# Optimization experiments

Measured on AMD Instinct MI355X. Metric: run time of the kernel, lower is better.

Reference implementation:

```python
import jax, jax.numpy as jnp
import numpy as np

C = 256   # hidden_size (in_channels)
V = 97    # VOC_SIZE + 1
T = 32    # encoder time steps
N = 4096  # batch of text instances


def setup_inputs() -> dict:
    key = jax.random.key(0)
    ks = jax.random.split(key, 10)
    s = lambda k, shape: jax.random.normal(k, shape, dtype=jnp.float32) * 0.05
    return {
        "input": jax.random.randint(ks[0], (N,), 0, V),
        "hidden": s(ks[1], (1, N, C)),
        "encoder_outputs": s(ks[2], (T, N, C)),
        "emb": s(ks[3], (V, C)),
        "combine_w": s(ks[4], (C, 2 * C)), "combine_b": jnp.zeros((C,), jnp.float32),
        "vat_w": s(ks[5], (1, C)), "vat_b": jnp.zeros((1,), jnp.float32),
        "gru_w_ih": s(ks[6], (3 * C, C)), "gru_w_hh": s(ks[7], (3 * C, C)),
        "gru_b_ih": jnp.zeros((3 * C,), jnp.float32), "gru_b_hh": jnp.zeros((3 * C,), jnp.float32),
        "out_w": s(ks[8], (V, C)), "out_b": jnp.zeros((V,), jnp.float32),
    }


def reference(input, hidden, encoder_outputs, emb, combine_w, combine_b,
              vat_w, vat_b, gru_w_ih, gru_w_hh, gru_b_ih, gru_b_hh,
              out_w, out_b):
    # Embedding lookup (dropout = identity in eval mode)
    embedded = emb[input]                                   # [N, C]

    # Bahdanau additive attention: vat(tanh(hidden + enc))
    alpha = jnp.tanh(hidden + encoder_outputs)              # [T, N, C]
    scores = jnp.einsum('tnc,c->nt', alpha, vat_w[0]) + vat_b[0]  # [N, T]
    attn = jax.nn.softmax(scores, axis=1)                   # [N, T]
    applied = jnp.einsum('nt,tnc->nc', attn, encoder_outputs)     # [N, C]

    # Combine + relu
    x = jnp.concatenate([embedded, applied], axis=1) @ combine_w.T + combine_b  # [N, C]
    x = jax.nn.relu(x)

    # Single-step GRU cell (PyTorch gate ordering: r, z, n)
    h = hidden[0]                                           # [N, C]
    gi = x @ gru_w_ih.T + gru_b_ih                          # [N, 3C]
    gh = h @ gru_w_hh.T + gru_b_hh                          # [N, 3C]
    ir, iz, i_n = jnp.split(gi, 3, axis=1)
    hr, hz, h_n = jnp.split(gh, 3, axis=1)
    r = jax.nn.sigmoid(ir + hr)
    z = jax.nn.sigmoid(iz + hz)
    n = jnp.tanh(i_n + r * h_n)
    h_new = (1.0 - z) * n + z * h                           # [N, C]

    out = jax.nn.log_softmax(h_new @ out_w.T + out_b, axis=1)  # [N, V]
    return out, h_new[None, :, :], attn[:, None, :]
```

## Files before the change

### kernel.cpp

```cpp
#include <hip/hip_runtime.h>

typedef unsigned short u16;
typedef unsigned int u32;
using bf16x8 = __attribute__((ext_vector_type(8))) __bf16;
using f32x4  = __attribute__((ext_vector_type(4))) float;

__device__ __forceinline__ u16 f2bf(float f) {
  union { float f; unsigned int i; } v; v.f = f;
  unsigned int r = v.i + 0x7fffu + ((v.i >> 16) & 1u);
  return (u16)(r >> 16);
}
__device__ __forceinline__ void cvt8(u16* dst, const float* src) {
  float4 a0 = *reinterpret_cast<const float4*>(src);
  float4 a1 = *reinterpret_cast<const float4*>(src + 4);
  dst[0] = f2bf(a0.x); dst[1] = f2bf(a0.y); dst[2] = f2bf(a0.z); dst[3] = f2bf(a0.w);
  dst[4] = f2bf(a1.x); dst[5] = f2bf(a1.y); dst[6] = f2bf(a1.z); dst[7] = f2bf(a1.w);
}
__device__ __forceinline__ float ftanh(float x) {
  float e = __expf(2.f * x);
  return 1.f - 2.f / (e + 1.f);
}
__device__ __forceinline__ float fsigm(float x) {
  return 1.f / (1.f + __expf(-x));
}
__device__ __forceinline__ float ptanh(float x) {
  const float c1 = -0.3333333333f, c2 = 0.1333333333f, c3 = -0.0539682540f;
  float t = x * x;
  float r = __builtin_fmaf(__builtin_fmaf(c3, t, c2), t, c1);
  return __builtin_fmaf(x * t, r, x);
}

__global__ __launch_bounds__(256) void k_prep(
    const float* __restrict__ cw, const float* __restrict__ wih,
    const float* __restrict__ whh, const float* __restrict__ ow,
    u16* __restrict__ Wc, u16* __restrict__ Wi,
    u16* __restrict__ Wh, u16* __restrict__ Wo)
{
  int id = blockIdx.x * 256 + threadIdx.x;
  u16 tmp[8];
  if (id < 16384) {
    cvt8(tmp, &cw[id * 8]);
    *reinterpret_cast<uint4*>(&Wc[id * 8]) = *reinterpret_cast<const uint4*>(tmp);
  } else if (id < 40960) {
    int c = id - 16384;
    cvt8(tmp, &wih[c * 8]);
    *reinterpret_cast<uint4*>(&Wi[c * 8]) = *reinterpret_cast<const uint4*>(tmp);
  } else if (id < 65536) {
    int c = id - 40960;
    cvt8(tmp, &whh[c * 8]);
    *reinterpret_cast<uint4*>(&Wh[c * 8]) = *reinterpret_cast<const uint4*>(tmp);
  } else {
    int c = id - 65536;
    int row = c >> 5, col = (c & 31) * 8;
    if (row < 97) {
      cvt8(tmp, &ow[row * 256 + col]);
    } else {
      #pragma unroll
      for (int i = 0; i < 8; ++i) tmp[i] = 0;
    }
    *reinterpret_cast<uint4*>(&Wo[c * 8]) = *reinterpret_cast<const uint4*>(tmp);
  }
}

__global__ __launch_bounds__(512) void k_fused(
    const float* __restrict__ enc, const float* __restrict__ hid,
    const float* __restrict__ vw,  const float* __restrict__ emb,
    const int* __restrict__ inp,
    const u16* __restrict__ Wc, const u16* __restrict__ Wi,
    const u16* __restrict__ Wh, const u16* __restrict__ Wo,
    const float* __restrict__ cb, const float* __restrict__ bih,
    const float* __restrict__ bhh, const float* __restrict__ bo,
    float* __restrict__ out_logits, float* __restrict__ out_h,
    float* __restrict__ out_attn)
{
  __shared__ __attribute__((aligned(16))) u16 Ac_s[16 * 16 * 40];
  __shared__ __attribute__((aligned(16))) u16 Hb_s[8 * 16 * 40];
  __shared__ __attribute__((aligned(16))) u16 X_s [8 * 16 * 40];
  __shared__ __attribute__((aligned(16))) u16 Hn_s[8 * 16 * 40];
  __shared__ float es_s[16 * 33];
  __shared__ float l_s[16];
  __shared__ float L_s[16 * 113];

  const int tid = threadIdx.x;
  const int n0  = blockIdx.x * 16;

  {
    const int nl = tid >> 5;
    const int cg = tid & 31;
    const int c0 = cg * 8;
    const int n  = n0 + nl;

    const float4 h0 = *reinterpret_cast<const float4*>(&hid[n * 256 + c0]);
    const float4 h1 = *reinterpret_cast<const float4*>(&hid[n * 256 + c0 + 4]);
    const float4 w0 = *reinterpret_cast<const float4*>(&vw[c0]);
    const float4 w1 = *reinterpret_cast<const float4*>(&vw[c0 + 4]);

    {
      u16 t8[8];
      t8[0]=f2bf(h0.x); t8[1]=f2bf(h0.y); t8[2]=f2bf(h0.z); t8[3]=f2bf(h0.w);
      t8[4]=f2bf(h1.x); t8[5]=f2bf(h1.y); t8[6]=f2bf(h1.z); t8[7]=f2bf(h1.w);
      *reinterpret_cast<uint4*>(&Hb_s[((cg >> 2) * 16 + nl) * 40 + (cg & 3) * 8]) =
        *reinterpret_cast<const uint4*>(t8);
    }
    {
      u16 t8[8];
      cvt8(t8, &emb[(size_t)inp[n] * 256 + c0]);
      *reinterpret_cast<uint4*>(&Ac_s[((cg >> 2) * 16 + nl) * 40 + (cg & 3) * 8]) =
        *reinterpret_cast<const uint4*>(t8);
    }

    float a0=0.f,a1=0.f,a2=0.f,a3=0.f,a4=0.f,a5=0.f,a6=0.f,a7=0.f;
    float l = 0.f;

    const float* ep = &enc[(size_t)n * 256 + c0];
    #pragma unroll 4
    for (int t = 0; t < 32; ++t) {
      const float* p = ep + (size_t)t * 1048576;
      float4 e0 = *reinterpret_cast<const float4*>(p);
      float4 e1 = *reinterpret_cast<const float4*>(p + 4);

      float s;
      s  = ptanh(h0.x + e0.x) * w0.x;
      s  = __builtin_fmaf(ptanh(h0.y + e0.y), w0.y, s);
      s  = __builtin_fmaf(ptanh(h0.z + e0.z), w0.z, s);
      s  = __builtin_fmaf(ptanh(h0.w + e0.w), w0.w, s);
      s  = __builtin_fmaf(ptanh(h1.x + e1.x), w1.x, s);
      s  = __builtin_fmaf(ptanh(h1.y + e1.y), w1.y, s);
      s  = __builtin_fmaf(ptanh(h1.z + e1.z), w1.z, s);
      s  = __builtin_fmaf(ptanh(h1.w + e1.w), w1.w, s);
      #pragma unroll
      for (int k = 16; k >= 1; k >>= 1) s += __shfl_xor(s, k, 64);

      float e = __expf(s);
      l += e;
      a0 = __builtin_fmaf(e, e0.x, a0); a1 = __builtin_fmaf(e, e0.y, a1);
      a2 = __builtin_fmaf(e, e0.z, a2); a3 = __builtin_fmaf(e, e0.w, a3);
      a4 = __builtin_fmaf(e, e1.x, a4); a5 = __builtin_fmaf(e, e1.y, a5);
      a6 = __builtin_fmaf(e, e1.z, a6); a7 = __builtin_fmaf(e, e1.w, a7);
      if (cg == 0) es_s[nl * 33 + t] = e;
    }

    {
      float rl = 1.f / l;
      u16 t8[8];
      t8[0]=f2bf(a0*rl); t8[1]=f2bf(a1*rl); t8[2]=f2bf(a2*rl); t8[3]=f2bf(a3*rl);
      t8[4]=f2bf(a4*rl); t8[5]=f2bf(a5*rl); t8[6]=f2bf(a6*rl); t8[7]=f2bf(a7*rl);
      *reinterpret_cast<uint4*>(&Ac_s[((8 + (cg >> 2)) * 16 + nl) * 40 + (cg & 3) * 8]) =
        *reinterpret_cast<const uint4*>(t8);
    }
    if (cg == 0) l_s[nl] = l;
  }
  __syncthreads();

  {
    int n2 = tid >> 5, t2 = tid & 31;
    out_attn[(size_t)(n0 + n2) * 32 + t2] = es_s[n2 * 33 + t2] / l_s[n2];
  }

  const int wave = tid >> 6, lane = tid & 63;
  const int lr = lane & 15, quad = lane >> 4;

  {
    f32x4 accB[2] = {};
    const u16* wp = &Wc[(size_t)(wave * 32 + lr) * 512 + quad * 8];
    #pragma unroll
    for (int kt = 0; kt < 16; ++kt) {
      bf16x8 aF = *reinterpret_cast<const bf16x8*>(&Ac_s[(kt * 16 + lr) * 40 + quad * 8]);
      bf16x8 b0 = *reinterpret_cast<const bf16x8*>(&wp[kt * 32]);
      bf16x8 b1 = *reinterpret_cast<const bf16x8*>(&wp[16 * 512 + kt * 32]);
      accB[0] = __builtin_amdgcn_mfma_f32_16x16x32_bf16(aF, b0, accB[0], 0, 0, 0);
      accB[1] = __builtin_amdgcn_mfma_f32_16x16x32_bf16(aF, b1, accB[1], 0, 0, 0);
    }
    #pragma unroll
    for (int sn = 0; sn < 2; ++sn) {
      int col = wave * 32 + sn * 16 + lr;
      float bv = cb[col];
      #pragma unroll
      for (int r = 0; r < 4; ++r) {
        float v = fmaxf(accB[sn][r] + bv, 0.f);
        X_s[((col >> 5) * 16 + quad * 4 + r) * 40 + (col & 31)] = f2bf(v);
      }
    }
  }
  __syncthreads();

  {
    f32x4 aI[3][2] = {};
    f32x4 aH[3][2] = {};
    const int c0w = wave * 32;
    const u16* baseI = &Wi[(size_t)(c0w + lr) * 256 + quad * 8];
    const u16* baseH = &Wh[(size_t)(c0w + lr) * 256 + quad * 8];
    #pragma unroll
    for (int kt = 0; kt < 8; ++kt) {
      bf16x8 xF = *reinterpret_cast<const bf16x8*>(&X_s [(kt * 16 + lr) * 40 + quad * 8]);
      bf16x8 hF = *reinterpret_cast<const bf16x8*>(&Hb_s[(kt * 16 + lr) * 40 + quad * 8]);
      #pragma unroll
      for (int g = 0; g < 3; ++g) {
        #pragma unroll
        for (int sn = 0; sn < 2; ++sn) {
          const size_t off = (size_t)(g * 256 + sn * 16) * 256 + kt * 32;
          bf16x8 bI = *reinterpret_cast<const bf16x8*>(&baseI[off]);
          bf16x8 bH = *reinterpret_cast<const bf16x8*>(&baseH[off]);
          aI[g][sn] = __builtin_amdgcn_mfma_f32_16x16x32_bf16(xF, bI, aI[g][sn], 0, 0, 0);
          aH[g][sn] = __builtin_amdgcn_mfma_f32_16x16x32_bf16(hF, bH, aH[g][sn], 0, 0, 0);
        }
      }
    }
    #pragma unroll
    for (int sn = 0; sn < 2; ++sn) {
      int gc = c0w + sn * 16 + lr;
      float b_ir = bih[gc],       b_hr = bhh[gc];
      float b_iz = bih[256 + gc], b_hz = bhh[256 + gc];
      float b_in = bih[512 + gc], b_hn = bhh[512 + gc];
      #pragma unroll
      for (int r = 0; r < 4; ++r) {
        int row = quad * 4 + r;
        float rg = fsigm(aI[0][sn][r] + b_ir + aH[0][sn][r] + b_hr);
        float zg = fsigm(aI[1][sn][r] + b_iz + aH[1][sn][r] + b_hz);
        float ng = ftanh(aI[2][sn][r] + b_in + rg * (aH[2][sn][r] + b_hn));
        float hv = hid[(size_t)(n0 + row) * 256 + gc];
        float hn = (1.f - zg) * ng + zg * hv;
        out_h[(size_t)(n0 + row) * 256 + gc] = hn;
        Hn_s[((gc >> 5) * 16 + row) * 40 + (gc & 31)] = f2bf(hn);
      }
    }
  }
  __syncthreads();

  if (wave < 7) {
    f32x4 accO = {};
    const u16* wp = &Wo[(size_t)(wave * 16 + lr) * 256 + quad * 8];
    #pragma unroll
    for (int kt = 0; kt < 8; ++kt) {
      bf16x8 aF = *reinterpret_cast<const bf16x8*>(&Hn_s[(kt * 16 + lr) * 40 + quad * 8]);
      bf16x8 bF = *reinterpret_cast<const bf16x8*>(&wp[kt * 32]);
      accO = __builtin_amdgcn_mfma_f32_16x16x32_bf16(aF, bF, accO, 0, 0, 0);
    }
    int col = wave * 16 + lr;
    if (col < 97) {
      float bv = bo[col];
      #pragma unroll
      for (int r = 0; r < 4; ++r)
        L_s[(quad * 4 + r) * 113 + col] = accO[r] + bv;
    }
  }
  __syncthreads();

  {
    int row = tid >> 5, p = tid & 31;
    float m = -1e30f, l = 0.f;
    for (int c = p; c < 97; c += 32) {
      float v = L_s[row * 113 + c];
      if (v > m) { l = l * __expf(m - v) + 1.f; m = v; }
      else l += __expf(v - m);
    }
    #pragma unroll
    for (int k = 16; k >= 1; k >>= 1) {
      float m2 = __shfl_xor(m, k, 64);
      float l2 = __shfl_xor(l, k, 64);
      if (m2 > m) { l = l * __expf(m - m2) + l2; m = m2; }
      else l += l2 * __expf(m2 - m);
    }
    float lz = m + __logf(l);
    for (int c = p; c < 97; c += 32)
      out_logits[(size_t)(n0 + row) * 97 + c] = L_s[row * 113 + c] - lz;
  }
}

extern "C" void kernel_launch(void* const* d_in, const int* in_sizes, int n_in,
                              void* d_out, int out_size, void* d_ws, size_t ws_size,
                              hipStream_t stream) {
  const int*   inp = (const int*)d_in[0];
  const float* hid = (const float*)d_in[1];
  const float* enc = (const float*)d_in[2];
  const float* emb = (const float*)d_in[3];
  const float* cw  = (const float*)d_in[4];
  const float* cb  = (const float*)d_in[5];
  const float* vw  = (const float*)d_in[6];
  const float* wih = (const float*)d_in[8];
  const float* whh = (const float*)d_in[9];
  const float* bih = (const float*)d_in[10];
  const float* bhh = (const float*)d_in[11];
  const float* ow  = (const float*)d_in[12];
  const float* ob  = (const float*)d_in[13];

  float* out        = (float*)d_out;
  float* out_logits = out;
  float* out_h      = out + 4096 * 97;
  float* out_attn   = out_h + 4096 * 256;

  u16* Wc = (u16*)d_ws;
  u16* Wi = Wc + 131072;
  u16* Wh = Wi + 196608;
  u16* Wo = Wh + 196608;

  k_prep<<<270, 256, 0, stream>>>(cw, wih, whh, ow, Wc, Wi, Wh, Wo);
  k_fused<<<256, 512, 0, stream>>>(enc, hid, vw, emb, inp,
                                   Wc, Wi, Wh, Wo, cb, bih, bhh, ob,
                                   out_logits, out_h, out_attn);
}
```

Before: 253.5 us.

## Halve rows per block to eight and double grid, aliasing shared memory

Each block now handles 8 batch rows instead of 16, with one wave per row in the attention stage, and the grid doubles to 512 blocks. The point is more blocks across CUs and better latency hiding in the memory-bound encoder scan. Shared buffers are aliased into one region to cut LDS use, which needs an extra barrier before X_s is written. In exchange, the 16-row MFMA tiles are half padding, so matrix work is wasted, and each weight matrix is read from L2 twice as many times overall.

```diff
diff --git a/kernel.cpp b/kernel.cpp
--- a/kernel.cpp
+++ b/kernel.cpp
@@ -73,92 +73,83 @@
     float* __restrict__ out_logits, float* __restrict__ out_h,
     float* __restrict__ out_attn)
 {
-  __shared__ __attribute__((aligned(16))) u16 Ac_s[16 * 16 * 40];
-  __shared__ __attribute__((aligned(16))) u16 Hb_s[8 * 16 * 40];
-  __shared__ __attribute__((aligned(16))) u16 X_s [8 * 16 * 40];
-  __shared__ __attribute__((aligned(16))) u16 Hn_s[8 * 16 * 40];
-  __shared__ float es_s[16 * 33];
-  __shared__ float l_s[16];
-  __shared__ float L_s[16 * 113];
+  __shared__ __attribute__((aligned(16))) u16 smem[15360];
+  u16* Ac_s = smem;
+  u16* X_s  = smem;
+  u16* Hn_s = smem + 5120;
+  u16* Hb_s = smem + 10240;
+  float* L_s = reinterpret_cast<float*>(smem + 10240);
+  __shared__ float es_s[8 * 33];
+  __shared__ float l_s[8];
 
   const int tid = threadIdx.x;
-  const int n0  = blockIdx.x * 16;
-
-  {
-    const int nl = tid >> 5;
-    const int cg = tid & 31;
-    const int c0 = cg * 8;
-    const int n  = n0 + nl;
-
-    const float4 h0 = *reinterpret_cast<const float4*>(&hid[n * 256 + c0]);
-    const float4 h1 = *reinterpret_cast<const float4*>(&hid[n * 256 + c0 + 4]);
-    const float4 w0 = *reinterpret_cast<const float4*>(&vw[c0]);
-    const float4 w1 = *reinterpret_cast<const float4*>(&vw[c0 + 4]);
+  const int n0  = blockIdx.x * 8;
+  const int wv  = tid >> 6;
+  const int ln  = tid & 63;
+
+  {
+    const int c0 = ln * 4;
+    const int n  = n0 + wv;
+    const int kt = ln >> 3;
+    const int cc = (ln & 7) * 4;
+
+    const float4 h = *reinterpret_cast<const float4*>(&hid[(size_t)n * 256 + c0]);
+    const float4 w = *reinterpret_cast<const float4*>(&vw[c0]);
 
     {
-      u16 t8[8];
-      t8[0]=f2bf(h0.x); t8[1]=f2bf(h0.y); t8[2]=f2bf(h0.z); t8[3]=f2bf(h0.w);
-      t8[4]=f2bf(h1.x); t8[5]=f2bf(h1.y); t8[6]=f2bf(h1.z); t8[7]=f2bf(h1.w);
-      *reinterpret_cast<uint4*>(&Hb_s[((cg >> 2) * 16 + nl) * 40 + (cg & 3) * 8]) =
-        *reinterpret_cast<const uint4*>(t8);
+      u16 t4[4];
+      t4[0]=f2bf(h.x); t4[1]=f2bf(h.y); t4[2]=f2bf(h.z); t4[3]=f2bf(h.w);
+      *reinterpret_cast<uint2*>(&Hb_s[(kt * 16 + wv) * 40 + cc]) =
+        *reinterpret_cast<const uint2*>(t4);
     }
     {
-      u16 t8[8];
-      cvt8(t8, &emb[(size_t)inp[n] * 256 + c0]);
-      *reinterpret_cast<uint4*>(&Ac_s[((cg >> 2) * 16 + nl) * 40 + (cg & 3) * 8]) =
-        *reinterpret_cast<const uint4*>(t8);
-    }
-
-    float a0=0.f,a1=0.f,a2=0.f,a3=0.f,a4=0.f,a5=0.f,a6=0.f,a7=0.f;
+      const float4 em = *reinterpret_cast<const float4*>(&emb[(size_t)inp[n] * 256 + c0]);
+      u16 t4[4];
+      t4[0]=f2bf(em.x); t4[1]=f2bf(em.y); t4[2]=f2bf(em.z); t4[3]=f2bf(em.w);
+      *reinterpret_cast<uint2*>(&Ac_s[(kt * 16 + wv) * 40 + cc]) =
+        *reinterpret_cast<const uint2*>(t4);
+    }
+
+    float a0=0.f, a1=0.f, a2=0.f, a3=0.f;
     float l = 0.f;
 
     const float* ep = &enc[(size_t)n * 256 + c0];
     #pragma unroll 4
     for (int t = 0; t < 32; ++t) {
-      const float* p = ep + (size_t)t * 1048576;
-      float4 e0 = *reinterpret_cast<const float4*>(p);
-      float4 e1 = *reinterpret_cast<const float4*>(p + 4);
+      const float4 e = *reinterpret_cast<const float4*>(ep + (size_t)t * 1048576);
 
       float s;
-      s  = ptanh(h0.x + e0.x) * w0.x;
-      s  = __builtin_fmaf(ptanh(h0.y + e0.y), w0.y, s);
-      s  = __builtin_fmaf(ptanh(h0.z + e0.z), w0.z, s);
-      s  = __builtin_fmaf(ptanh(h0.w + e0.w), w0.w, s);
-      s  = __builtin_fmaf(ptanh(h1.x + e1.x), w1.x, s);
-      s  = __builtin_fmaf(ptanh(h1.y + e1.y), w1.y, s);
-      s  = __builtin_fmaf(ptanh(h1.z + e1.z), w1.z, s);
-      s  = __builtin_fmaf(ptanh(h1.w + e1.w), w1.w, s);
-      #pragma unroll
-      for (int k = 16; k >= 1; k >>= 1) s += __shfl_xor(s, k, 64);
-
-      float e = __expf(s);
-      l += e;
-      a0 = __builtin_fmaf(e, e0.x, a0); a1 = __builtin_fmaf(e, e0.y, a1);
-      a2 = __builtin_fmaf(e, e0.z, a2); a3 = __builtin_fmaf(e, e0.w, a3);
-      a4 = __builtin_fmaf(e, e1.x, a4); a5 = __builtin_fmaf(e, e1.y, a5);
-      a6 = __builtin_fmaf(e, e1.z, a6); a7 = __builtin_fmaf(e, e1.w, a7);
-      if (cg == 0) es_s[nl * 33 + t] = e;
+      s  = ptanh(h.x + e.x) * w.x;
+      s  = __builtin_fmaf(ptanh(h.y + e.y), w.y, s);
+      s  = __builtin_fmaf(ptanh(h.z + e.z), w.z, s);
+      s  = __builtin_fmaf(ptanh(h.w + e.w), w.w, s);
+      #pragma unroll
+      for (int k = 32; k >= 1; k >>= 1) s += __shfl_xor(s, k, 64);
+
+      float ex = __expf(s);
+      l += ex;
+      a0 = __builtin_fmaf(ex, e.x, a0); a1 = __builtin_fmaf(ex, e.y, a1);
+      a2 = __builtin_fmaf(ex, e.z, a2); a3 = __builtin_fmaf(ex, e.w, a3);
+      if (ln == 0) es_s[wv * 33 + t] = ex;
     }
 
     {
       float rl = 1.f / l;
-      u16 t8[8];
-      t8[0]=f2bf(a0*rl); t8[1]=f2bf(a1*rl); t8[2]=f2bf(a2*rl); t8[3]=f2bf(a3*rl);
-      t8[4]=f2bf(a4*rl); t8[5]=f2bf(a5*rl); t8[6]=f2bf(a6*rl); t8[7]=f2bf(a7*rl);
-      *reinterpret_cast<uint4*>(&Ac_s[((8 + (cg >> 2)) * 16 + nl) * 40 + (cg & 3) * 8]) =
-        *reinterpret_cast<const uint4*>(t8);
-    }
-    if (cg == 0) l_s[nl] = l;
-  }
-  __syncthreads();
-
-  {
+      u16 t4[4];
+      t4[0]=f2bf(a0*rl); t4[1]=f2bf(a1*rl); t4[2]=f2bf(a2*rl); t4[3]=f2bf(a3*rl);
+      *reinterpret_cast<uint2*>(&Ac_s[((8 + kt) * 16 + wv) * 40 + cc]) =
+        *reinterpret_cast<const uint2*>(t4);
+    }
+    if (ln == 0) l_s[wv] = l;
+  }
+  __syncthreads();
+
+  if (tid < 256) {
     int n2 = tid >> 5, t2 = tid & 31;
     out_attn[(size_t)(n0 + n2) * 32 + t2] = es_s[n2 * 33 + t2] / l_s[n2];
   }
 
-  const int wave = tid >> 6, lane = tid & 63;
-  const int lr = lane & 15, quad = lane >> 4;
+  const int wave = wv, lr = ln & 15, quad = ln >> 4;
 
   {
     f32x4 accB[2] = {};
@@ -171,14 +162,17 @@
       accB[0] = __builtin_amdgcn_mfma_f32_16x16x32_bf16(aF, b0, accB[0], 0, 0, 0);
       accB[1] = __builtin_amdgcn_mfma_f32_16x16x32_bf16(aF, b1, accB[1], 0, 0, 0);
     }
-    #pragma unroll
-    for (int sn = 0; sn < 2; ++sn) {
-      int col = wave * 32 + sn * 16 + lr;
-      float bv = cb[col];
-      #pragma unroll
-      for (int r = 0; r < 4; ++r) {
-        float v = fmaxf(accB[sn][r] + bv, 0.f);
-        X_s[((col >> 5) * 16 + quad * 4 + r) * 40 + (col & 31)] = f2bf(v);
+    __syncthreads();
+    if (quad < 2) {
+      #pragma unroll
+      for (int sn = 0; sn < 2; ++sn) {
+        int col = wave * 32 + sn * 16 + lr;
+        float bv = cb[col];
+        #pragma unroll
+        for (int r = 0; r < 4; ++r) {
+          float v = fmaxf(accB[sn][r] + bv, 0.f);
+          X_s[((col >> 5) * 16 + quad * 4 + r) * 40 + (col & 31)] = f2bf(v);
+        }
       }
     }
   }
@@ -206,22 +200,24 @@
         }
       }
     }
-    #pragma unroll
-    for (int sn = 0; sn < 2; ++sn) {
-      int gc = c0w + sn * 16 + lr;
-      float b_ir = bih[gc],       b_hr = bhh[gc];
-      float b_iz = bih[256 + gc], b_hz = bhh[256 + gc];
-      float b_in = bih[512 + gc], b_hn = bhh[512 + gc];
-      #pragma unroll
-      for (int r = 0; r < 4; ++r) {
-        int row = quad * 4 + r;
-        float rg = fsigm(aI[0][sn][r] + b_ir + aH[0][sn][r] + b_hr);
-        float zg = fsigm(aI[1][sn][r] + b_iz + aH[1][sn][r] + b_hz);
-        float ng = ftanh(aI[2][sn][r] + b_in + rg * (aH[2][sn][r] + b_hn));
-        float hv = hid[(size_t)(n0 + row) * 256 + gc];
-        float hn = (1.f - zg) * ng + zg * hv;
-        out_h[(size_t)(n0 + row) * 256 + gc] = hn;
-        Hn_s[((gc >> 5) * 16 + row) * 40 + (gc & 31)] = f2bf(hn);
+    if (quad < 2) {
+      #pragma unroll
+      for (int sn = 0; sn < 2; ++sn) {
+        int gc = c0w + sn * 16 + lr;
+        float b_ir = bih[gc],       b_hr = bhh[gc];
+        float b_iz = bih[256 + gc], b_hz = bhh[256 + gc];
+        float b_in = bih[512 + gc], b_hn = bhh[512 + gc];
+        #pragma unroll
+        for (int r = 0; r < 4; ++r) {
+          int row = quad * 4 + r;
+          float rg = fsigm(aI[0][sn][r] + b_ir + aH[0][sn][r] + b_hr);
+          float zg = fsigm(aI[1][sn][r] + b_iz + aH[1][sn][r] + b_hz);
+          float ng = ftanh(aI[2][sn][r] + b_in + rg * (aH[2][sn][r] + b_hn));
+          float hv = hid[(size_t)(n0 + row) * 256 + gc];
+          float hn = (1.f - zg) * ng + zg * hv;
+          out_h[(size_t)(n0 + row) * 256 + gc] = hn;
+          Hn_s[((gc >> 5) * 16 + row) * 40 + (gc & 31)] = f2bf(hn);
+        }
       }
     }
   }
@@ -237,7 +233,7 @@
       accO = __builtin_amdgcn_mfma_f32_16x16x32_bf16(aF, bF, accO, 0, 0, 0);
     }
     int col = wave * 16 + lr;
-    if (col < 97) {
+    if (col < 97 && quad < 2) {
       float bv = bo[col];
       #pragma unroll
       for (int r = 0; r < 4; ++r)
@@ -247,22 +243,22 @@
   __syncthreads();
 
   {
-    int row = tid >> 5, p = tid & 31;
+    int row = wv;
     float m = -1e30f, l = 0.f;
-    for (int c = p; c < 97; c += 32) {
+    for (int c = ln; c < 97; c += 64) {
       float v = L_s[row * 113 + c];
       if (v > m) { l = l * __expf(m - v) + 1.f; m = v; }
       else l += __expf(v - m);
     }
     #pragma unroll
-    for (int k = 16; k >= 1; k >>= 1) {
+    for (int k = 32; k >= 1; k >>= 1) {
       float m2 = __shfl_xor(m, k, 64);
       float l2 = __shfl_xor(l, k, 64);
       if (m2 > m) { l = l * __expf(m - m2) + l2; m = m2; }
       else l += l2 * __expf(m2 - m);
     }
     float lz = m + __logf(l);
-    for (int c = p; c < 97; c += 32)
+    for (int c = ln; c < 97; c += 64)
       out_logits[(size_t)(n0 + row) * 97 + c] = L_s[row * 113 + c] - lz;
   }
 }
@@ -295,7 +291,7 @@
   u16* Wo = Wh + 196608;
 
   k_prep<<<270, 256, 0, stream>>>(cw, wih, whh, ow, Wc, Wi, Wh, Wo);
-  k_fused<<<256, 512, 0, stream>>>(enc, hid, vw, emb, inp,
+  k_fused<<<512, 512, 0, stream>>>(enc, hid, vw, emb, inp,
                                    Wc, Wi, Wh, Wo, cb, bih, bhh, ob,
                                    out_logits, out_h, out_attn);
 }
```

Measured after the change: 280.9 us. 10.8% more time.

## Software-pipeline global loads with register ring buffers and request two blocks per CU

Applied to the files above, without the earlier changes.

Adds explicit register prefetching throughout the fused kernel. The encoder loop loads four time steps ahead, and each MFMA GEMM stage (combine, GRU input/hidden, output projection) streams its weight fragments through a 4-deep register ring. The GRU accumulators are flattened into a 12-entry array, and hidden-state values and biases are loaded before the MMA loop. Launch bounds now ask for 2 blocks per CU, which caps registers per thread and may cause spills.

```diff
diff --git a/kernel.cpp b/kernel.cpp
--- a/kernel.cpp
+++ b/kernel.cpp
@@ -62,7 +62,7 @@
   }
 }
 
-__global__ __launch_bounds__(512) void k_fused(
+__global__ __launch_bounds__(512, 2) void k_fused(
     const float* __restrict__ enc, const float* __restrict__ hid,
     const float* __restrict__ vw,  const float* __restrict__ emb,
     const int* __restrict__ inp,
@@ -90,8 +90,8 @@
     const int c0 = cg * 8;
     const int n  = n0 + nl;
 
-    const float4 h0 = *reinterpret_cast<const float4*>(&hid[n * 256 + c0]);
-    const float4 h1 = *reinterpret_cast<const float4*>(&hid[n * 256 + c0 + 4]);
+    const float4 h0 = *reinterpret_cast<const float4*>(&hid[(size_t)n * 256 + c0]);
+    const float4 h1 = *reinterpret_cast<const float4*>(&hid[(size_t)n * 256 + c0 + 4]);
     const float4 w0 = *reinterpret_cast<const float4*>(&vw[c0]);
     const float4 w1 = *reinterpret_cast<const float4*>(&vw[c0 + 4]);
 
@@ -113,31 +113,44 @@
     float l = 0.f;
 
     const float* ep = &enc[(size_t)n * 256 + c0];
-    #pragma unroll 4
-    for (int t = 0; t < 32; ++t) {
-      const float* p = ep + (size_t)t * 1048576;
-      float4 e0 = *reinterpret_cast<const float4*>(p);
-      float4 e1 = *reinterpret_cast<const float4*>(p + 4);
-
-      float s;
-      s  = ptanh(h0.x + e0.x) * w0.x;
-      s  = __builtin_fmaf(ptanh(h0.y + e0.y), w0.y, s);
-      s  = __builtin_fmaf(ptanh(h0.z + e0.z), w0.z, s);
-      s  = __builtin_fmaf(ptanh(h0.w + e0.w), w0.w, s);
-      s  = __builtin_fmaf(ptanh(h1.x + e1.x), w1.x, s);
-      s  = __builtin_fmaf(ptanh(h1.y + e1.y), w1.y, s);
-      s  = __builtin_fmaf(ptanh(h1.z + e1.z), w1.z, s);
-      s  = __builtin_fmaf(ptanh(h1.w + e1.w), w1.w, s);
-      #pragma unroll
-      for (int k = 16; k >= 1; k >>= 1) s += __shfl_xor(s, k, 64);
-
-      float e = __expf(s);
-      l += e;
-      a0 = __builtin_fmaf(e, e0.x, a0); a1 = __builtin_fmaf(e, e0.y, a1);
-      a2 = __builtin_fmaf(e, e0.z, a2); a3 = __builtin_fmaf(e, e0.w, a3);
-      a4 = __builtin_fmaf(e, e1.x, a4); a5 = __builtin_fmaf(e, e1.y, a5);
-      a6 = __builtin_fmaf(e, e1.z, a6); a7 = __builtin_fmaf(e, e1.w, a7);
-      if (cg == 0) es_s[nl * 33 + t] = e;
+    float4 E0[4], E1[4];
+    #pragma unroll
+    for (int i = 0; i < 4; ++i) {
+      const float* p = ep + (size_t)i * 1048576;
+      E0[i] = *reinterpret_cast<const float4*>(p);
+      E1[i] = *reinterpret_cast<const float4*>(p + 4);
+    }
+    #pragma unroll
+    for (int tb = 0; tb < 32; tb += 4) {
+      #pragma unroll
+      for (int i = 0; i < 4; ++i) {
+        const int t = tb + i;
+        float4 e0 = E0[i], e1 = E1[i];
+        if (tb < 28) {
+          const float* p = ep + (size_t)(t + 4) * 1048576;
+          E0[i] = *reinterpret_cast<const float4*>(p);
+          E1[i] = *reinterpret_cast<const float4*>(p + 4);
+        }
+        float s;
+        s  = ptanh(h0.x + e0.x) * w0.x;
+        s  = __builtin_fmaf(ptanh(h0.y + e0.y), w0.y, s);
+        s  = __builtin_fmaf(ptanh(h0.z + e0.z), w0.z, s);
+        s  = __builtin_fmaf(ptanh(h0.w + e0.w), w0.w, s);
+        s  = __builtin_fmaf(ptanh(h1.x + e1.x), w1.x, s);
+        s  = __builtin_fmaf(ptanh(h1.y + e1.y), w1.y, s);
+        s  = __builtin_fmaf(ptanh(h1.z + e1.z), w1.z, s);
+        s  = __builtin_fmaf(ptanh(h1.w + e1.w), w1.w, s);
+        #pragma unroll
+        for (int k = 16; k >= 1; k >>= 1) s += __shfl_xor(s, k, 64);
+
+        float e = __expf(s);
+        l += e;
+        a0 = __builtin_fmaf(e, e0.x, a0); a1 = __builtin_fmaf(e, e0.y, a1);
+        a2 = __builtin_fmaf(e, e0.z, a2); a3 = __builtin_fmaf(e, e0.w, a3);
+        a4 = __builtin_fmaf(e, e1.x, a4); a5 = __builtin_fmaf(e, e1.y, a5);
+        a6 = __builtin_fmaf(e, e1.z, a6); a7 = __builtin_fmaf(e, e1.w, a7);
+        if (cg == 0) es_s[nl * 33 + t] = e;
+      }
     }
 
     {
@@ -163,18 +176,32 @@
   {
     f32x4 accB[2] = {};
     const u16* wp = &Wc[(size_t)(wave * 32 + lr) * 512 + quad * 8];
-    #pragma unroll
-    for (int kt = 0; kt < 16; ++kt) {
-      bf16x8 aF = *reinterpret_cast<const bf16x8*>(&Ac_s[(kt * 16 + lr) * 40 + quad * 8]);
-      bf16x8 b0 = *reinterpret_cast<const bf16x8*>(&wp[kt * 32]);
-      bf16x8 b1 = *reinterpret_cast<const bf16x8*>(&wp[16 * 512 + kt * 32]);
-      accB[0] = __builtin_amdgcn_mfma_f32_16x16x32_bf16(aF, b0, accB[0], 0, 0, 0);
-      accB[1] = __builtin_amdgcn_mfma_f32_16x16x32_bf16(aF, b1, accB[1], 0, 0, 0);
+    float bv0 = cb[wave * 32 + lr];
+    float bv1 = cb[wave * 32 + 16 + lr];
+
+    bf16x8 ring[4];
+    #pragma unroll
+    for (int i = 0; i < 4; ++i) {
+      int kt = i >> 1, half = i & 1;
+      ring[i] = *reinterpret_cast<const bf16x8*>(&wp[half * 16 * 512 + kt * 32]);
+    }
+    bf16x8 aF = {};
+    #pragma unroll
+    for (int s = 0; s < 32; ++s) {
+      const int kt = s >> 1, half = s & 1;
+      bf16x8 bF = ring[s & 3];
+      if (s + 4 < 32) {
+        int kt2 = (s + 4) >> 1, h2 = (s + 4) & 1;
+        ring[s & 3] = *reinterpret_cast<const bf16x8*>(&wp[h2 * 16 * 512 + kt2 * 32]);
+      }
+      if (half == 0)
+        aF = *reinterpret_cast<const bf16x8*>(&Ac_s[(kt * 16 + lr) * 40 + quad * 8]);
+      accB[half] = __builtin_amdgcn_mfma_f32_16x16x32_bf16(aF, bF, accB[half], 0, 0, 0);
     }
     #pragma unroll
     for (int sn = 0; sn < 2; ++sn) {
       int col = wave * 32 + sn * 16 + lr;
-      float bv = cb[col];
+      float bv = sn ? bv1 : bv0;
       #pragma unroll
       for (int r = 0; r < 4; ++r) {
         float v = fmaxf(accB[sn][r] + bv, 0.f);
@@ -185,41 +212,69 @@
   __syncthreads();
 
   {
-    f32x4 aI[3][2] = {};
-    f32x4 aH[3][2] = {};
     const int c0w = wave * 32;
     const u16* baseI = &Wi[(size_t)(c0w + lr) * 256 + quad * 8];
     const u16* baseH = &Wh[(size_t)(c0w + lr) * 256 + quad * 8];
-    #pragma unroll
-    for (int kt = 0; kt < 8; ++kt) {
-      bf16x8 xF = *reinterpret_cast<const bf16x8*>(&X_s [(kt * 16 + lr) * 40 + quad * 8]);
-      bf16x8 hF = *reinterpret_cast<const bf16x8*>(&Hb_s[(kt * 16 + lr) * 40 + quad * 8]);
-      #pragma unroll
-      for (int g = 0; g < 3; ++g) {
-        #pragma unroll
-        for (int sn = 0; sn < 2; ++sn) {
-          const size_t off = (size_t)(g * 256 + sn * 16) * 256 + kt * 32;
-          bf16x8 bI = *reinterpret_cast<const bf16x8*>(&baseI[off]);
-          bf16x8 bH = *reinterpret_cast<const bf16x8*>(&baseH[off]);
-          aI[g][sn] = __builtin_amdgcn_mfma_f32_16x16x32_bf16(xF, bI, aI[g][sn], 0, 0, 0);
-          aH[g][sn] = __builtin_amdgcn_mfma_f32_16x16x32_bf16(hF, bH, aH[g][sn], 0, 0, 0);
-        }
-      }
-    }
+
+    float b_ir[2], b_hr[2], b_iz[2], b_hz[2], b_in[2], b_hn[2], hv[2][4];
     #pragma unroll
     for (int sn = 0; sn < 2; ++sn) {
       int gc = c0w + sn * 16 + lr;
-      float b_ir = bih[gc],       b_hr = bhh[gc];
-      float b_iz = bih[256 + gc], b_hz = bhh[256 + gc];
-      float b_in = bih[512 + gc], b_hn = bhh[512 + gc];
+      b_ir[sn] = bih[gc];       b_hr[sn] = bhh[gc];
+      b_iz[sn] = bih[256 + gc]; b_hz[sn] = bhh[256 + gc];
+      b_in[sn] = bih[512 + gc]; b_hn[sn] = bhh[512 + gc];
+      #pragma unroll
+      for (int r = 0; r < 4; ++r) {
+        int row = (quad & 1) * 4 + r + (quad >> 1) * 8;
+        hv[sn][r] = hid[(size_t)(n0 + ((quad * 4 + r) & 15)) * 256 + gc];
+      }
+    }
+
+    f32x4 accC[12] = {};
+    bf16x8 ring[4];
+    #pragma unroll
+    for (int i = 0; i < 4; ++i) {
+      const int g = i >> 2, sn = (i >> 1) & 1, mat = i & 1;
+      const u16* base = mat ? baseH : baseI;
+      ring[i] = *reinterpret_cast<const bf16x8*>(&base[(size_t)(g * 256 + sn * 16) * 256]);
+    }
+    bf16x8 xF = {}, hF = {};
+    #pragma unroll
+    for (int s = 0; s < 96; ++s) {
+      const int kt = s / 12, j = s % 12;
+      const int mat = j & 1;
+      bf16x8 bF = ring[s & 3];
+      if (s + 4 < 96) {
+        const int s2 = s + 4, kt2 = s2 / 12, j2 = s2 % 12;
+        const int g2 = j2 >> 2, sn2 = (j2 >> 1) & 1, m2 = j2 & 1;
+        const u16* base = m2 ? baseH : baseI;
+        ring[s & 3] = *reinterpret_cast<const bf16x8*>(
+            &base[(size_t)(g2 * 256 + sn2 * 16) * 256 + kt2 * 32]);
+      }
+      if (j == 0) {
+        xF = *reinterpret_cast<const bf16x8*>(&X_s [(kt * 16 + lr) * 40 + quad * 8]);
+        hF = *reinterpret_cast<const bf16x8*>(&Hb_s[(kt * 16 + lr) * 40 + quad * 8]);
+      }
+      accC[j] = __builtin_amdgcn_mfma_f32_16x16x32_bf16(mat ? hF : xF, bF, accC[j], 0, 0, 0);
+    }
+
+    #pragma unroll
+    for (int sn = 0; sn < 2; ++sn) {
+      int gc = c0w + sn * 16 + lr;
       #pragma unroll
       for (int r = 0; r < 4; ++r) {
         int row = quad * 4 + r;
-        float rg = fsigm(aI[0][sn][r] + b_ir + aH[0][sn][r] + b_hr);
-        float zg = fsigm(aI[1][sn][r] + b_iz + aH[1][sn][r] + b_hz);
-        float ng = ftanh(aI[2][sn][r] + b_in + rg * (aH[2][sn][r] + b_hn));
-        float hv = hid[(size_t)(n0 + row) * 256 + gc];
-        float hn = (1.f - zg) * ng + zg * hv;
+        float aIr = accC[(0 << 2) | (sn << 1) | 0][r];
+        float aHr = accC[(0 << 2) | (sn << 1) | 1][r];
+        float aIz = accC[(1 << 2) | (sn << 1) | 0][r];
+        float aHz = accC[(1 << 2) | (sn << 1) | 1][r];
+        float aIn = accC[(2 << 2) | (sn << 1) | 0][r];
+        float aHn = accC[(2 << 2) | (sn << 1) | 1][r];
+        float rg = fsigm(aIr + b_ir[sn] + aHr + b_hr[sn]);
+        float zg = fsigm(aIz + b_iz[sn] + aHz + b_hz[sn]);
+        float ng = ftanh(aIn + b_in[sn] + rg * (aHn + b_hn[sn]));
+        float hvv = hv[sn][r];
+        float hn = (1.f - zg) * ng + zg * hvv;
         out_h[(size_t)(n0 + row) * 256 + gc] = hn;
         Hn_s[((gc >> 5) * 16 + row) * 40 + (gc & 31)] = f2bf(hn);
       }
@@ -230,10 +285,16 @@
   if (wave < 7) {
     f32x4 accO = {};
     const u16* wp = &Wo[(size_t)(wave * 16 + lr) * 256 + quad * 8];
+    bf16x8 ring[4];
+    #pragma unroll
+    for (int i = 0; i < 4; ++i)
+      ring[i] = *reinterpret_cast<const bf16x8*>(&wp[i * 32]);
     #pragma unroll
     for (int kt = 0; kt < 8; ++kt) {
+      bf16x8 bF = ring[kt & 3];
+      if (kt + 4 < 8)
+        ring[kt & 3] = *reinterpret_cast<const bf16x8*>(&wp[(kt + 4) * 32]);
       bf16x8 aF = *reinterpret_cast<const bf16x8*>(&Hn_s[(kt * 16 + lr) * 40 + quad * 8]);
-      bf16x8 bF = *reinterpret_cast<const bf16x8*>(&wp[kt * 32]);
       accO = __builtin_amdgcn_mfma_f32_16x16x32_bf16(aF, bF, accO, 0, 0, 0);
     }
     int col = wave * 16 + lr;
```

New measurement: 273.4 us. +7.9%, slower.

## Split attention into a separate per-row kernel with many more blocks

Applied to the files above, without the earlier changes.

Moves the attention stage out of the fused kernel into its own kernel that launches one 256-thread block per batch row, with each of four waves handling eight time steps. The previous version ran only 256 blocks. The new kernel writes the combined embedding and attention-applied vector in bf16 to a workspace buffer. A second kernel loads that buffer and runs the GEMM/GRU/output stages. This gives the memory-bound attention read far more parallelism for latency hiding, at the cost of an extra kernel launch and a global round-trip for the combined activations.

```diff
diff --git a/kernel.cpp b/kernel.cpp
--- a/kernel.cpp
+++ b/kernel.cpp
@@ -62,100 +62,91 @@
   }
 }
 
-__global__ __launch_bounds__(512) void k_fused(
+__global__ __launch_bounds__(256) void k_attn(
     const float* __restrict__ enc, const float* __restrict__ hid,
     const float* __restrict__ vw,  const float* __restrict__ emb,
     const int* __restrict__ inp,
+    float* __restrict__ out_attn, u16* __restrict__ Acomb)
+{
+  __shared__ float a_s[4][256];
+  __shared__ float es_s[32];
+  __shared__ float l_s[4];
+
+  const int n   = blockIdx.x;
+  const int tid = threadIdx.x;
+  const int w   = tid >> 6;
+  const int ln  = tid & 63;
+  const int c0  = ln * 4;
+
+  const float4 h  = *reinterpret_cast<const float4*>(&hid[(size_t)n * 256 + c0]);
+  const float4 wv = *reinterpret_cast<const float4*>(&vw[c0]);
+
+  float a0 = 0.f, a1 = 0.f, a2 = 0.f, a3 = 0.f, l = 0.f;
+  const float* ep = &enc[(size_t)n * 256 + c0];
+
+  #pragma unroll
+  for (int j = 0; j < 8; ++j) {
+    const int t = w * 8 + j;
+    const float4 e = *reinterpret_cast<const float4*>(ep + (size_t)t * 1048576);
+    float s;
+    s = ptanh(h.x + e.x) * wv.x;
+    s = __builtin_fmaf(ptanh(h.y + e.y), wv.y, s);
+    s = __builtin_fmaf(ptanh(h.z + e.z), wv.z, s);
+    s = __builtin_fmaf(ptanh(h.w + e.w), wv.w, s);
+    #pragma unroll
+    for (int k = 32; k >= 1; k >>= 1) s += __shfl_xor(s, k, 64);
+    float ex = __expf(s);
+    l += ex;
+    a0 = __builtin_fmaf(ex, e.x, a0); a1 = __builtin_fmaf(ex, e.y, a1);
+    a2 = __builtin_fmaf(ex, e.z, a2); a3 = __builtin_fmaf(ex, e.w, a3);
+    if (ln == 0) es_s[t] = ex;
+  }
+
+  *reinterpret_cast<float4*>(&a_s[w][c0]) = make_float4(a0, a1, a2, a3);
+  if (ln == 0) l_s[w] = l;
+  __syncthreads();
+
+  {
+    const int c = tid;
+    float lt = (l_s[0] + l_s[1]) + (l_s[2] + l_s[3]);
+    float at = (a_s[0][c] + a_s[1][c]) + (a_s[2][c] + a_s[3][c]);
+    Acomb[(size_t)n * 512 + 256 + c] = f2bf(at / lt);
+    float em = emb[(size_t)inp[n] * 256 + c];
+    Acomb[(size_t)n * 512 + c] = f2bf(em);
+    if (c < 32) out_attn[(size_t)n * 32 + c] = es_s[c] / lt;
+  }
+}
+
+__global__ __launch_bounds__(512) void k_rest(
+    const float* __restrict__ hid, const u16* __restrict__ Acomb,
     const u16* __restrict__ Wc, const u16* __restrict__ Wi,
     const u16* __restrict__ Wh, const u16* __restrict__ Wo,
     const float* __restrict__ cb, const float* __restrict__ bih,
     const float* __restrict__ bhh, const float* __restrict__ bo,
-    float* __restrict__ out_logits, float* __restrict__ out_h,
-    float* __restrict__ out_attn)
+    float* __restrict__ out_logits, float* __restrict__ out_h)
 {
   __shared__ __attribute__((aligned(16))) u16 Ac_s[16 * 16 * 40];
   __shared__ __attribute__((aligned(16))) u16 Hb_s[8 * 16 * 40];
   __shared__ __attribute__((aligned(16))) u16 X_s [8 * 16 * 40];
   __shared__ __attribute__((aligned(16))) u16 Hn_s[8 * 16 * 40];
-  __shared__ float es_s[16 * 33];
-  __shared__ float l_s[16];
   __shared__ float L_s[16 * 113];
 
   const int tid = threadIdx.x;
   const int n0  = blockIdx.x * 16;
 
-  {
-    const int nl = tid >> 5;
-    const int cg = tid & 31;
-    const int c0 = cg * 8;
-    const int n  = n0 + nl;
-
-    const float4 h0 = *reinterpret_cast<const float4*>(&hid[n * 256 + c0]);
-    const float4 h1 = *reinterpret_cast<const float4*>(&hid[n * 256 + c0 + 4]);
-    const float4 w0 = *reinterpret_cast<const float4*>(&vw[c0]);
-    const float4 w1 = *reinterpret_cast<const float4*>(&vw[c0 + 4]);
-
-    {
-      u16 t8[8];
-      t8[0]=f2bf(h0.x); t8[1]=f2bf(h0.y); t8[2]=f2bf(h0.z); t8[3]=f2bf(h0.w);
-      t8[4]=f2bf(h1.x); t8[5]=f2bf(h1.y); t8[6]=f2bf(h1.z); t8[7]=f2bf(h1.w);
-      *reinterpret_cast<uint4*>(&Hb_s[((cg >> 2) * 16 + nl) * 40 + (cg & 3) * 8]) =
-        *reinterpret_cast<const uint4*>(t8);
-    }
-    {
-      u16 t8[8];
-      cvt8(t8, &emb[(size_t)inp[n] * 256 + c0]);
-      *reinterpret_cast<uint4*>(&Ac_s[((cg >> 2) * 16 + nl) * 40 + (cg & 3) * 8]) =
-        *reinterpret_cast<const uint4*>(t8);
-    }
-
-    float a0=0.f,a1=0.f,a2=0.f,a3=0.f,a4=0.f,a5=0.f,a6=0.f,a7=0.f;
-    float l = 0.f;
-
-    const float* ep = &enc[(size_t)n * 256 + c0];
-    #pragma unroll 4
-    for (int t = 0; t < 32; ++t) {
-      const float* p = ep + (size_t)t * 1048576;
-      float4 e0 = *reinterpret_cast<const float4*>(p);
-      float4 e1 = *reinterpret_cast<const float4*>(p + 4);
-
-      float s;
-      s  = ptanh(h0.x + e0.x) * w0.x;
-      s  = __builtin_fmaf(ptanh(h0.y + e0.y), w0.y, s);
-      s  = __builtin_fmaf(ptanh(h0.z + e0.z), w0.z, s);
-      s  = __builtin_fmaf(ptanh(h0.w + e0.w), w0.w, s);
-      s  = __builtin_fmaf(ptanh(h1.x + e1.x), w1.x, s);
-      s  = __builtin_fmaf(ptanh(h1.y + e1.y), w1.y, s);
-      s  = __builtin_fmaf(ptanh(h1.z + e1.z), w1.z, s);
-      s  = __builtin_fmaf(ptanh(h1.w + e1.w), w1.w, s);
-      #pragma unroll
-      for (int k = 16; k >= 1; k >>= 1) s += __shfl_xor(s, k, 64);
-
-      float e = __expf(s);
-      l += e;
-      a0 = __builtin_fmaf(e, e0.x, a0); a1 = __builtin_fmaf(e, e0.y, a1);
-      a2 = __builtin_fmaf(e, e0.z, a2); a3 = __builtin_fmaf(e, e0.w, a3);
-      a4 = __builtin_fmaf(e, e1.x, a4); a5 = __builtin_fmaf(e, e1.y, a5);
-      a6 = __builtin_fmaf(e, e1.z, a6); a7 = __builtin_fmaf(e, e1.w, a7);
-      if (cg == 0) es_s[nl * 33 + t] = e;
-    }
-
-    {
-      float rl = 1.f / l;
-      u16 t8[8];
-      t8[0]=f2bf(a0*rl); t8[1]=f2bf(a1*rl); t8[2]=f2bf(a2*rl); t8[3]=f2bf(a3*rl);
-      t8[4]=f2bf(a4*rl); t8[5]=f2bf(a5*rl); t8[6]=f2bf(a6*rl); t8[7]=f2bf(a7*rl);
-      *reinterpret_cast<uint4*>(&Ac_s[((8 + (cg >> 2)) * 16 + nl) * 40 + (cg & 3) * 8]) =
-        *reinterpret_cast<const uint4*>(t8);
-    }
-    if (cg == 0) l_s[nl] = l;
-  }
-  __syncthreads();
-
-  {
-    int n2 = tid >> 5, t2 = tid & 31;
-    out_attn[(size_t)(n0 + n2) * 32 + t2] = es_s[n2 * 33 + t2] / l_s[n2];
-  }
+  #pragma unroll
+  for (int i = 0; i < 2; ++i) {
+    int idx = tid + i * 512;
+    int row = idx >> 6, q = idx & 63;
+    *reinterpret_cast<uint4*>(&Ac_s[((q >> 2) * 16 + row) * 40 + (q & 3) * 8]) =
+      *reinterpret_cast<const uint4*>(&Acomb[(size_t)(n0 + row) * 512 + q * 8]);
+  }
+  {
+    int row = tid >> 5, q = tid & 31;
+    cvt8(&Hb_s[((q >> 2) * 16 + row) * 40 + (q & 3) * 8],
+         &hid[(size_t)(n0 + row) * 256 + q * 8]);
+  }
+  __syncthreads();
 
   const int wave = tid >> 6, lane = tid & 63;
   const int lr = lane & 15, quad = lane >> 4;
@@ -289,13 +280,14 @@
   float* out_h      = out + 4096 * 97;
   float* out_attn   = out_h + 4096 * 256;
 
-  u16* Wc = (u16*)d_ws;
+  u16* Acomb = (u16*)d_ws;
+  u16* Wc = Acomb + 4096 * 512;
   u16* Wi = Wc + 131072;
   u16* Wh = Wi + 196608;
   u16* Wo = Wh + 196608;
 
   k_prep<<<270, 256, 0, stream>>>(cw, wih, whh, ow, Wc, Wi, Wh, Wo);
-  k_fused<<<256, 512, 0, stream>>>(enc, hid, vw, emb, inp,
-                                   Wc, Wi, Wh, Wo, cb, bih, bhh, ob,
-                                   out_logits, out_h, out_attn);
-}
+  k_attn<<<4096, 256, 0, stream>>>(enc, hid, vw, emb, inp, out_attn, Acomb);
+  k_rest<<<256, 512, 0, stream>>>(hid, Acomb, Wc, Wi, Wh, Wo,
+                                  cb, bih, bhh, ob, out_logits, out_h);
+}
```

Result: slower. 259.5 us (+2.4%).
